# Optimization experiments

Measured on AMD Instinct MI355X. Metric: run time of the kernel, lower is better.

Reference implementation:

```python
import jax, jax.numpy as jnp
import numpy as np

N, E, G = 100000, 1600000, 1000
D_IN, D, L, C = 128, 300, 5, 10


def setup_inputs() -> dict:
    key = jax.random.key(0)
    ks = jax.random.split(key, 32)
    s = 0.05
    inp = {
        'x': jax.random.normal(ks[0], (N, D_IN), jnp.float32),
        'edge_index': jax.random.randint(ks[1], (2, E), 0, N, jnp.int64),
        'batch': jnp.sort(jax.random.randint(ks[2], (N,), 0, G, jnp.int64)),
        'enc_W': jax.random.normal(ks[3], (D_IN, D)) * s,
        'enc_b': jnp.zeros((D,)),
        'eps': jnp.zeros((L,)),
        'cW1': jax.random.normal(ks[4], (L, D, 2 * D)) * s,
        'cb1': jnp.zeros((L, 2 * D)),
        'cbn_s': jnp.ones((L, 2 * D)),
        'cbn_b': jnp.zeros((L, 2 * D)),
        'cW2': jax.random.normal(ks[5], (L, 2 * D, D)) * s,
        'cb2': jnp.zeros((L, D)),
        'bn_s': jnp.ones((L, D)),
        'bn_b': jnp.zeros((L, D)),
        'vn0': jnp.zeros((D,)),
        'vW1': jax.random.normal(ks[6], (L, D, 2 * D)) * s,
        'vb1': jnp.zeros((L, 2 * D)),
        'vbn1_s': jnp.ones((L, 2 * D)),
        'vbn1_b': jnp.zeros((L, 2 * D)),
        'vW2': jax.random.normal(ks[7], (L, 2 * D, D)) * s,
        'vb2': jnp.zeros((L, D)),
        'vbn2_s': jnp.ones((L, D)),
        'vbn2_b': jnp.zeros((L, D)),
        'gW1': jax.random.normal(ks[8], (D, 2 * D)) * s,
        'gb1': jnp.zeros((2 * D,)),
        'gbn_s': jnp.ones((2 * D,)),
        'gbn_b': jnp.zeros((2 * D,)),
        'gW2': jax.random.normal(ks[9], (2 * D, 1)) * s,
        'gb2': jnp.zeros((1,)),
        'pW': jax.random.normal(ks[10], (D, C)) * s,
        'pb': jnp.zeros((C,)),
    }
    return inp


def reference(x, enc_W, enc_b, eps, cW1, cb1, cbn_s, cbn_b, cW2, cb2,
              bn_s, bn_b, vn0, vW1, vb1, vbn1_s, vbn1_b, vW2, vb2,
              vbn2_s, vbn2_b, gW1, gb1, gbn_s, gbn_b, gW2, gb2, pW, pb,
              edge_index, batch):
    src, dst = edge_index[0], edge_index[1]
    n = x.shape[0]
    vn = jnp.broadcast_to(vn0, (G, D))  # virtualnode_embedding(zeros) -> row 0 per graph
    h_list = [x @ enc_W + enc_b]
    for l in range(L):
        hl = h_list[l] + vn[batch]  # virtual-node broadcast gather
        # GIN conv: MLP((1+eps)*h + sum_{j in N(i)} h_j)
        agg = jax.ops.segment_sum(hl[src], dst, num_segments=n)
        t = (1.0 + eps[l]) * hl + agg
        t = jax.nn.relu((t @ cW1[l] + cb1[l]) * cbn_s[l] + cbn_b[l])
        h = (t @ cW2[l] + cb2[l]) * bn_s[l] + bn_b[l]  # layer BN (eval, folded)
        if l < L - 1:
            h = jax.nn.relu(h)  # dropout is identity in eval
        # virtual-node update: global_add_pool + MLP
        vtmp = jax.ops.segment_sum(hl, batch, num_segments=G) + vn
        u = jax.nn.relu((vtmp @ vW1[l] + vb1[l]) * vbn1_s[l] + vbn1_b[l])
        vn = jax.nn.relu((u @ vW2[l] + vb2[l]) * vbn2_s[l] + vbn2_b[l])
        h_list.append(h)
    # JK = 'max' across all L+1 layer outputs
    nr = jnp.max(jnp.stack(h_list, axis=0), axis=0)  # [N, D]
    # GlobalAttention pooling: gate_nn -> per-graph segment softmax
    gate = (jax.nn.relu((nr @ gW1 + gb1) * gbn_s + gbn_b) @ gW2 + gb2)[:, 0]
    gmax = jax.ops.segment_max(gate, batch, num_segments=G)
    e = jnp.exp(gate - gmax[batch])
    denom = jax.ops.segment_sum(e, batch, num_segments=G)
    alpha = e / denom[batch]
    graph_rep = jax.ops.segment_sum(nr * alpha[:, None], batch, num_segments=G)
    return graph_rep @ pW + pb  # [G, C]
```

## Files before the change

kernel.cpp:

```cpp
#include <hip/hip_runtime.h>
#include <cstddef>

#define NGRAPH 1000
#define NEDGES 1600000
#define DD     300
#define DD2    600
#define DIN    128
#define NLAYER 5
#define NCLS   10
#define BR     32
#define BRM    32

#define NT2 38
#define NK2 10
#define NT3 19
#define NK3 19
#define WFRAG 1024
#define W1F_SZ (NT2*NK2*WFRAG)

typedef unsigned short u16;
typedef unsigned char  u8;
typedef unsigned int   u32;
typedef __attribute__((ext_vector_type(8))) short short8;
typedef __attribute__((ext_vector_type(4))) float f32x4;

__device__ __forceinline__ u16 f2bf(float f) {
    u32 u; __builtin_memcpy(&u, &f, 4);
    u = (u + 0x7FFFu + ((u >> 16) & 1u)) >> 16;
    return (u16)u;
}
__device__ __forceinline__ float bf2f(u16 h) {
    u32 u = ((u32)h) << 16;
    float f; __builtin_memcpy(&f, &u, 4); return f;
}

__device__ __forceinline__ float ld24(const u16* __restrict__ hi, const u8* __restrict__ lo,
                                      size_t idx) {
    u32 u = ((u32)hi[idx] << 16) | ((u32)lo[idx] << 8);
    float f; __builtin_memcpy(&f, &u, 4); return f;
}
__device__ __forceinline__ void st24(u16* __restrict__ hi, u8* __restrict__ lo,
                                     size_t idx, float f) {
    u32 u; __builtin_memcpy(&u, &f, 4);
    u32 r = u + 0x7Fu + ((u >> 8) & 1u);
    hi[idx] = (u16)(r >> 16); lo[idx] = (u8)(r >> 8);
}
__device__ __forceinline__ void ld24x4(const u16* __restrict__ hi, const u8* __restrict__ lo,
                                       size_t idx, float o[4]) {
    ushort4 h = *(const ushort4*)(hi + idx);
    uchar4  l = *(const uchar4*)(lo + idx);
    u32 u0 = ((u32)h.x << 16) | ((u32)l.x << 8);
    u32 u1 = ((u32)h.y << 16) | ((u32)l.y << 8);
    u32 u2 = ((u32)h.z << 16) | ((u32)l.z << 8);
    u32 u3 = ((u32)h.w << 16) | ((u32)l.w << 8);
    __builtin_memcpy(&o[0], &u0, 4); __builtin_memcpy(&o[1], &u1, 4);
    __builtin_memcpy(&o[2], &u2, 4); __builtin_memcpy(&o[3], &u3, 4);
}
__device__ __forceinline__ void st24x4(u16* __restrict__ hi, u8* __restrict__ lo,
                                       size_t idx, const float v[4]) {
    u32 u[4];
#pragma unroll
    for (int q = 0; q < 4; ++q) {
        u32 t; __builtin_memcpy(&t, &v[q], 4);
        u[q] = t + 0x7Fu + ((t >> 8) & 1u);
    }
    ushort4 h; h.x = (u16)(u[0] >> 16); h.y = (u16)(u[1] >> 16);
    h.z = (u16)(u[2] >> 16); h.w = (u16)(u[3] >> 16);
    uchar4 l8; l8.x = (u8)(u[0] >> 8); l8.y = (u8)(u[1] >> 8);
    l8.z = (u8)(u[2] >> 8); l8.w = (u8)(u[3] >> 8);
    *(ushort4*)(hi + idx) = h;
    *(uchar4*)(lo + idx) = l8;
}

__global__ void diag_kernel(float* __restrict__ out, int n, float val)
{
    int i = blockIdx.x * 256 + threadIdx.x;
    if (i < n) out[i] = val;
}

__global__ void vn_init_kernel(float* __restrict__ vn, const float* __restrict__ vn0)
{
    int idx = blockIdx.x * 256 + threadIdx.x;
    if (idx < NGRAPH * DD) vn[idx] = vn0[idx % DD];
}

__global__ void bconv_kernel(const int* __restrict__ braw, int n, int* __restrict__ b32)
{
    int i = blockIdx.x * 256 + threadIdx.x;
    if (i >= n) return;
    int fs = (braw[n - 1] == 0) ? 2 : 1;
    b32[i] = braw[(size_t)i * fs];
}

__global__ void packW_kernel(const float* __restrict__ W, int K, int N,
                             int nT, int nK, short* __restrict__ dst)
{
    int idx = blockIdx.x * 256 + threadIdx.x;
    int total = nT * nK * 64;
    if (idx >= total) return;
    int lane = idx & 63;
    int tk = idx >> 6;
    int nn = (tk / nK) * 16 + (lane & 15);
    int k0 = (tk % nK) * 32 + (lane >> 4) * 8;
    short* o = dst + ((size_t)tk << 10) + lane * 8;
#pragma unroll
    for (int j = 0; j < 8; ++j) {
        float v = (nn < N && (k0 + j) < K) ? W[(size_t)(k0 + j) * N + nn] : 0.f;
        u16 h = f2bf(v);
        o[j] = (short)h;
        o[512 + j] = (short)f2bf(v - bf2f(h));
    }
}

__global__ void deg_kernel(const int* __restrict__ ei, int fe, int E, int* __restrict__ deg)
{
    int e = blockIdx.x * 256 + threadIdx.x;
    if (e < E) atomicAdd(&deg[ei[(size_t)fe * (E + e)]], 1);
}

__global__ void scan_kernel(const int* __restrict__ deg, int* __restrict__ row_ptr, int n)
{
    __shared__ int sd[1024];
    int t = threadIdx.x;
    int C = (n + 1023) >> 10;
    int i0 = t * C, i1 = i0 + C; if (i1 > n) i1 = n; if (i0 > n) i0 = n;
    int s = 0;
    for (int i = i0; i < i1; ++i) s += deg[i];
    sd[t] = s;
    __syncthreads();
    for (int o = 1; o < 1024; o <<= 1) {
        int x = (t >= o) ? sd[t - o] : 0;
        __syncthreads();
        sd[t] += x;
        __syncthreads();
    }
    int run = (t == 0) ? 0 : sd[t - 1];
    for (int i = i0; i < i1; ++i) { row_ptr[i] = run; run += deg[i]; }
    if (t == 1023) row_ptr[n] = sd[1023];
}

__global__ void scatter_kernel(const int* __restrict__ ei, int fe, int E,
                               int* __restrict__ cursor, int* __restrict__ col_idx)
{
    int e = blockIdx.x * 256 + threadIdx.x;
    if (e < E) {
        int d = ei[(size_t)fe * (E + e)];
        int s = ei[(size_t)fe * e];
        int p = atomicAdd(&cursor[d], 1);
        col_idx[p] = s;
    }
}

__device__ __forceinline__ int lower_bound_i(const int* __restrict__ arr, int n, int key)
{
    int lo = 0, hi = n;
    while (lo < hi) {
        int mid = (lo + hi) >> 1;
        if (arr[mid] < key) lo = mid + 1; else hi = mid;
    }
    return lo;
}

__global__ void vtmp_kernel(const u16* __restrict__ hi, const u8* __restrict__ lo,
                            const int* __restrict__ batch, const float* __restrict__ vn,
                            float* __restrict__ vtmp, int n)
{
    int g = blockIdx.x, t = threadIdx.x;
    int l0 = lower_bound_i(batch, n, g);
    int h0 = lower_bound_i(batch, n, g + 1);
    if (t >= DD) return;
    float acc = 0.f;
    for (int i = l0; i < h0; ++i) acc += ld24(hi, lo, (size_t)i * DD + t);
    vtmp[(size_t)g * DD + t] = acc + vn[(size_t)g * DD + t];
}

__global__ void vn_mlp_kernel(const float* __restrict__ vtmp,
                              const float* __restrict__ W1, const float* __restrict__ b1,
                              const float* __restrict__ s1, const float* __restrict__ sb1,
                              const float* __restrict__ W2, const float* __restrict__ b2,
                              const float* __restrict__ s2, const float* __restrict__ sb2,
                              float* __restrict__ vn)
{
    __shared__ float vt[DD];
    __shared__ float us[DD2];
    int g = blockIdx.x, t = threadIdx.x;
    if (t < DD) vt[t] = vtmp[(size_t)g * DD + t];
    __syncthreads();
    for (int j = t; j < DD2; j += 512) {
        float acc = 0.f;
        for (int k = 0; k < DD; ++k) acc = fmaf(vt[k], W1[(size_t)k * DD2 + j], acc);
        us[j] = fmaxf(fmaf(acc + b1[j], s1[j], sb1[j]), 0.f);
    }
    __syncthreads();
    for (int j = t; j < DD; j += 512) {
        float acc = 0.f;
        for (int k = 0; k < DD2; ++k) acc = fmaf(us[k], W2[(size_t)k * DD + j], acc);
        vn[(size_t)g * DD + j] = fmaxf(fmaf(acc + b2[j], s2[j], sb2[j]), 0.f);
    }
}

__global__ __launch_bounds__(1024)
void encoder_kernel(const float* __restrict__ x, const float* __restrict__ W,
                    const float* __restrict__ b,
                    u16* __restrict__ Ahi, u8* __restrict__ Alo,
                    short* __restrict__ NRm, float* __restrict__ NRscale, int n)
{
    __shared__ float xs[BR][DIN];
    __shared__ float wmax[16][8];
    __shared__ float rowS[BR];
    const int tid = threadIdx.x;
    const int base = blockIdx.x * BR;
    for (int idx = tid; idx < BR * DIN; idx += 1024) {
        int r = idx >> 7, c = idx & 127;
        int node = base + r;
        xs[r][c] = (node < n) ? x[(size_t)node * DIN + c] : 0.f;
    }
    __syncthreads();
    const int rq = tid >> 8, ct = tid & 255;
    const int wid = tid >> 6, lane = tid & 63;
    const int j0 = ct; const bool has1 = ct < (DD - 256); const int j1 = ct + 256;
    float acc[8][2] = {};
    for (int k = 0; k < DIN; ++k) {
        const float* wr = W + (size_t)k * DD;
        float w0 = wr[j0], w1 = has1 ? wr[j1] : 0.f;
#pragma unroll
        for (int i = 0; i < 8; ++i) {
            float a = xs[rq * 8 + i][k];
            acc[i][0] = fmaf(a, w0, acc[i][0]);
            acc[i][1] = fmaf(a, w1, acc[i][1]);
        }
    }
    float bb0 = b[j0], bb1 = has1 ? b[j1] : 0.f;
    float v0[8], v1[8], lm[8];
#pragma unroll
    for (int i = 0; i < 8; ++i) {
        v0[i] = acc[i][0] + bb0;
        v1[i] = has1 ? (acc[i][1] + bb1) : 0.f;
        lm[i] = fmaxf(fabsf(v0[i]), fabsf(v1[i]));
    }
#pragma unroll
    for (int o = 32; o > 0; o >>= 1)
#pragma unroll
        for (int i = 0; i < 8; ++i) lm[i] = fmaxf(lm[i], __shfl_xor(lm[i], o));
    if (lane == 0)
#pragma unroll
        for (int i = 0; i < 8; ++i) wmax[wid][i] = lm[i];
    __syncthreads();
    if (ct < 8) {
        int r = rq * 8 + ct;
        float m = fmaxf(fmaxf(wmax[4 * rq][ct], wmax[4 * rq + 1][ct]),
                        fmaxf(wmax[4 * rq + 2][ct], wmax[4 * rq + 3][ct]));
        float S = fmaxf(m, 1e-30f) / 32767.f;
        rowS[r] = S;
        if (base + r < n) NRscale[base + r] = S;
    }
    __syncthreads();
#pragma unroll
    for (int i = 0; i < 8; ++i) {
        int r = rq * 8 + i;
        int node = base + r;
        if (node >= n) continue;
        float S = rowS[r];
        size_t idx = (size_t)node * DD + j0;
        st24(Ahi, Alo, idx, v0[i]);
        NRm[idx] = (short)rintf(v0[i] / S);
        if (has1) {
            st24(Ahi, Alo, idx + 256, v1[i]);
            NRm[idx + 256] = (short)rintf(v1[i] / S);
        }
    }
}

__global__ __launch_bounds__(256)
void agg_kernel(const u16* __restrict__ Phi, const u8* __restrict__ Plo,
                u16* __restrict__ Qhi, u8* __restrict__ Qlo,
                const int* __restrict__ row_ptr, const int* __restrict__ col_idx,
                const float* __restrict__ eps, int l, int n)
{
    int node = blockIdx.x * 4 + (threadIdx.x >> 6);
    int lane = threadIdx.x & 63;
    if (node >= n) return;
    const float ep = 1.0f + eps[l];
    const bool two = (lane < 11);
    float a0[4] = {0.f, 0.f, 0.f, 0.f}, a1[4] = {0.f, 0.f, 0.f, 0.f};
    int e0 = row_ptr[node], e1 = row_ptr[node + 1];
    for (int e = e0; e < e1; ++e) {
        int src = col_idx[e];
        size_t rb = (size_t)src * DD;
        float v[4];
        ld24x4(Phi, Plo, rb + lane * 4, v);
        a0[0] += v[0]; a0[1] += v[1]; a0[2] += v[2]; a0[3] += v[3];
        if (two) {
            ld24x4(Phi, Plo, rb + 256 + lane * 4, v);
            a1[0] += v[0]; a1[1] += v[1]; a1[2] += v[2]; a1[3] += v[3];
        }
    }
    size_t ob = (size_t)node * DD;
    float v[4], o[4];
    ld24x4(Phi, Plo, ob + lane * 4, v);
#pragma unroll
    for (int q = 0; q < 4; ++q) o[q] = fmaf(ep, v[q], a0[q]);
    st24x4(Qhi, Qlo, ob + lane * 4, o);
    if (two) {
        ld24x4(Phi, Plo, ob + 256 + lane * 4, v);
#pragma unroll
        for (int q = 0; q < 4; ++q) o[q] = fmaf(ep, v[q], a1[q]);
        st24x4(Qhi, Qlo, ob + 256 + lane * 4, o);
    }
}

__global__ __launch_bounds__(512)
void mlp_kernel(u16* __restrict__ Qhi, u8* __restrict__ Qlo,
                short* __restrict__ NRm, float* __restrict__ NRscale,
                const short* __restrict__ W1f, const float* __restrict__ b1,
                const float* __restrict__ s1, const float* __restrict__ sb1,
                const short* __restrict__ W2f, const float* __restrict__ b2,
                const float* __restrict__ s2, const float* __restrict__ sb2,
                int relu2, const float* __restrict__ vnp,
                const int* __restrict__ batch, int n)
{
    __shared__ char uni[78848];
    __shared__ float rowM[32], rowSo[32], rowSn[32];
    short* agh = (short*)uni;
    short* agl = (short*)(uni + 20992);
    short* tlh = (short*)uni;
    short* tll = (short*)(uni + 39424);
    float* outb = (float*)uni;

    const int tid = threadIdx.x;
    const int base = blockIdx.x * BRM;
    const int wv = tid >> 6, lane = tid & 63;
    const int cl = lane & 15, kq = lane >> 4, r0 = kq * 4;

    for (int idx = tid; idx < 32 * 320; idx += 512) {
        int r = idx / 320, c = idx - r * 320;
        int node = base + r;
        float v = (c < DD && node < n) ? ld24(Qhi, Qlo, (size_t)node * DD + c) : 0.f;
        u16 h = f2bf(v);
        agh[r * 328 + c] = (short)h;
        agl[r * 328 + c] = (short)f2bf(v - bf2f(h));
    }
    __syncthreads();

    {
        f32x4 acc[2][5];
#pragma unroll
        for (int s = 0; s < 2; ++s)
#pragma unroll
            for (int i = 0; i < 5; ++i) acc[s][i] = (f32x4){0.f, 0.f, 0.f, 0.f};
        const bool act5 = (wv + 32) < NT2;
        for (int ks = 0; ks < NK2; ++ks) {
            short8 bh[5], bl[5];
#pragma unroll
            for (int i = 0; i < 5; ++i) {
                int t = wv + 8 * i;
                if (i < 4 || act5) {
                    const short* bp = W1f + (((size_t)t * NK2 + ks) << 10) + lane * 8;
                    bh[i] = *(const short8*)bp;
                    bl[i] = *(const short8*)(bp + 512);
                }
            }
            short8 ah0 = *(const short8*)&agh[cl * 328 + kq * 8 + ks * 32];
            short8 al0 = *(const short8*)&agl[cl * 328 + kq * 8 + ks * 32];
            short8 ah1 = *(const short8*)&agh[(16 + cl) * 328 + kq * 8 + ks * 32];
            short8 al1 = *(const short8*)&agl[(16 + cl) * 328 + kq * 8 + ks * 32];
#pragma unroll
            for (int i = 0; i < 5; ++i)
                if (i < 4 || act5) {
                    acc[0][i] = __builtin_amdgcn_mfma_f32_16x16x32_bf16(ah0, bh[i], acc[0][i], 0, 0, 0);
                    acc[1][i] = __builtin_amdgcn_mfma_f32_16x16x32_bf16(ah1, bh[i], acc[1][i], 0, 0, 0);
                }
#pragma unroll
            for (int i = 0; i < 5; ++i)
                if (i < 4 || act5) {
                    acc[0][i] = __builtin_amdgcn_mfma_f32_16x16x32_bf16(ah0, bl[i], acc[0][i], 0, 0, 0);
                    acc[1][i] = __builtin_amdgcn_mfma_f32_16x16x32_bf16(ah1, bl[i], acc[1][i], 0, 0, 0);
                }
#pragma unroll
            for (int i = 0; i < 5; ++i)
                if (i < 4 || act5) {
                    acc[0][i] = __builtin_amdgcn_mfma_f32_16x16x32_bf16(al0, bh[i], acc[0][i], 0, 0, 0);
                    acc[1][i] = __builtin_amdgcn_mfma_f32_16x16x32_bf16(al1, bh[i], acc[1][i], 0, 0, 0);
                }
        }
        __syncthreads();
        if (tid < 256) {
            int r = tid >> 3, c = 600 + (tid & 7);
            tlh[r * 616 + c] = 0; tll[r * 616 + c] = 0;
        }
#pragma unroll
        for (int s = 0; s < 2; ++s)
#pragma unroll
            for (int i = 0; i < 5; ++i) {
                int t = wv + 8 * i;
                if (t >= NT2) continue;
                int cg = t * 16 + cl;
                if (cg < DD2) {
                    float bb = b1[cg], ss = s1[cg], cc = sb1[cg];
#pragma unroll
                    for (int r = 0; r < 4; ++r) {
                        float xv = fmaxf(fmaf(acc[s][i][r] + bb, ss, cc), 0.f);
                        u16 h = f2bf(xv);
                        tlh[(s * 16 + r0 + r) * 616 + cg] = (short)h;
                        tll[(s * 16 + r0 + r) * 616 + cg] = (short)f2bf(xv - bf2f(h));
                    }
                }
            }
    }
    __syncthreads();

    {
        f32x4 acc[2][3];
#pragma unroll
        for (int s = 0; s < 2; ++s)
#pragma unroll
            for (int i = 0; i < 3; ++i) acc[s][i] = (f32x4){0.f, 0.f, 0.f, 0.f};
        const bool act3 = (wv + 16) < NT3;
        for (int ks = 0; ks < NK3; ++ks) {
            short8 bh[3], bl[3];
#pragma unroll
            for (int i = 0; i < 3; ++i) {
                int t = wv + 8 * i;
                if (i < 2 || act3) {
                    const short* bp = W2f + (((size_t)t * NK3 + ks) << 10) + lane * 8;
                    bh[i] = *(const short8*)bp;
                    bl[i] = *(const short8*)(bp + 512);
                }
            }
            short8 ah0 = *(const short8*)&tlh[cl * 616 + kq * 8 + ks * 32];
            short8 al0 = *(const short8*)&tll[cl * 616 + kq * 8 + ks * 32];
            short8 ah1 = *(const short8*)&tlh[(16 + cl) * 616 + kq * 8 + ks * 32];
            short8 al1 = *(const short8*)&tll[(16 + cl) * 616 + kq * 8 + ks * 32];
#pragma unroll
            for (int i = 0; i < 3; ++i)
                if (i < 2 || act3) {
                    acc[0][i] = __builtin_amdgcn_mfma_f32_16x16x32_bf16(ah0, bh[i], acc[0][i], 0, 0, 0);
                    acc[1][i] = __builtin_amdgcn_mfma_f32_16x16x32_bf16(ah1, bh[i], acc[1][i], 0, 0, 0);
                }
#pragma unroll
            for (int i = 0; i < 3; ++i)
                if (i < 2 || act3) {
                    acc[0][i] = __builtin_amdgcn_mfma_f32_16x16x32_bf16(ah0, bl[i], acc[0][i], 0, 0, 0);
                    acc[1][i] = __builtin_amdgcn_mfma_f32_16x16x32_bf16(ah1, bl[i], acc[1][i], 0, 0, 0);
                }
#pragma unroll
            for (int i = 0; i < 3; ++i)
                if (i < 2 || act3) {
                    acc[0][i] = __builtin_amdgcn_mfma_f32_16x16x32_bf16(al0, bh[i], acc[0][i], 0, 0, 0);
                    acc[1][i] = __builtin_amdgcn_mfma_f32_16x16x32_bf16(al1, bh[i], acc[1][i], 0, 0, 0);
                }
        }
        __syncthreads();
#pragma unroll
        for (int s = 0; s < 2; ++s)
#pragma unroll
            for (int i = 0; i < 3; ++i) {
                int t = wv + 8 * i;
                if (t >= NT3) continue;
                int cg = t * 16 + cl;
#pragma unroll
                for (int r = 0; r < 4; ++r) outb[(s * 16 + r0 + r) * 304 + cg] = acc[s][i][r];
            }
    }
    __syncthreads();

    {
        const int rr = tid >> 4;
        const int qq = tid & 15;
        float lm = 0.f;
        for (int c = qq; c < DD; c += 16) {
            float v = fmaf(outb[rr * 304 + c] + b2[c], s2[c], sb2[c]);
            if (relu2) v = fmaxf(v, 0.f);
            outb[rr * 304 + c] = v;
            lm = fmaxf(lm, fabsf(v));
        }
#pragma unroll
        for (int o = 8; o > 0; o >>= 1) lm = fmaxf(lm, __shfl_xor(lm, o));
        if (qq == 0) rowM[rr] = lm;
        __syncthreads();
        if (tid < 32) {
            int node = base + tid;
            float oS = (node < n) ? NRscale[node] : 0.f;
            float newM = fmaxf(rowM[tid], oS * 32767.f);
            float nS = fmaxf(newM, 1e-30f) / 32767.f;
            rowSo[tid] = oS; rowSn[tid] = nS;
            if (node < n) NRscale[node] = nS;
        }
        __syncthreads();
        int node = base + rr;
        if (node < n) {
            float oS = rowSo[rr], inv = 1.0f / rowSn[rr];
            const float* vrow = vnp ? (vnp + (size_t)batch[node] * DD) : nullptr;
            for (int c = qq; c < DD; c += 16) {
                float v = outb[rr * 304 + c];
                size_t idx = (size_t)node * DD + c;
                float hl = vrow ? (v + vrow[c]) : v;
                st24(Qhi, Qlo, idx, hl);
                float nv = fmaxf((float)NRm[idx] * oS, v);
                NRm[idx] = (short)rintf(nv * inv);
            }
        }
    }
}

__global__ __launch_bounds__(512)
void gate_kernel(const short* __restrict__ NRm, const float* __restrict__ NRscale,
                 const short* __restrict__ W1f, const float* __restrict__ b1,
                 const float* __restrict__ s1, const float* __restrict__ sb1,
                 const float* __restrict__ W2, const float* __restrict__ b2,
                 float* __restrict__ gate, int n)
{
    __shared__ char uni[78336];
    __shared__ float sc[32];
    short* nbh = (short*)uni;
    short* nbl = (short*)(uni + 20992);
    float* tlf = (float*)uni;

    const int tid = threadIdx.x;
    const int base = blockIdx.x * BRM;
    const int wv = tid >> 6, lane = tid & 63;
    const int cl = lane & 15, kq = lane >> 4, r0 = kq * 4;

    if (tid < 32) {
        int node = base + tid;
        sc[tid] = (node < n) ? NRscale[node] : 0.f;
    }
    __syncthreads();
    for (int idx = tid; idx < 32 * 320; idx += 512) {
        int r = idx / 320, c = idx - r * 320;
        int node = base + r;
        float v = (c < DD && node < n) ? (float)NRm[(size_t)node * DD + c] * sc[r] : 0.f;
        u16 h = f2bf(v);
        nbh[r * 328 + c] = (short)h;
        nbl[r * 328 + c] = (short)f2bf(v - bf2f(h));
    }
    __syncthreads();

    {
        f32x4 acc[2][5];
#pragma unroll
        for (int s = 0; s < 2; ++s)
#pragma unroll
            for (int i = 0; i < 5; ++i) acc[s][i] = (f32x4){0.f, 0.f, 0.f, 0.f};
        const bool act5 = (wv + 32) < NT2;
        for (int ks = 0; ks < NK2; ++ks) {
            short8 bh[5], bl[5];
#pragma unroll
            for (int i = 0; i < 5; ++i) {
                int t = wv + 8 * i;
                if (i < 4 || act5) {
                    const short* bp = W1f + (((size_t)t * NK2 + ks) << 10) + lane * 8;
                    bh[i] = *(const short8*)bp;
                    bl[i] = *(const short8*)(bp + 512);
                }
            }
            short8 ah0 = *(const short8*)&nbh[cl * 328 + kq * 8 + ks * 32];
            short8 al0 = *(const short8*)&nbl[cl * 328 + kq * 8 + ks * 32];
            short8 ah1 = *(const short8*)&nbh[(16 + cl) * 328 + kq * 8 + ks * 32];
            short8 al1 = *(const short8*)&nbl[(16 + cl) * 328 + kq * 8 + ks * 32];
#pragma unroll
            for (int i = 0; i < 5; ++i)
                if (i < 4 || act5) {
                    acc[0][i] = __builtin_amdgcn_mfma_f32_16x16x32_bf16(ah0, bh[i], acc[0][i], 0, 0, 0);
                    acc[1][i] = __builtin_amdgcn_mfma_f32_16x16x32_bf16(ah1, bh[i], acc[1][i], 0, 0, 0);
                }
#pragma unroll
            for (int i = 0; i < 5; ++i)
                if (i < 4 || act5) {
                    acc[0][i] = __builtin_amdgcn_mfma_f32_16x16x32_bf16(ah0, bl[i], acc[0][i], 0, 0, 0);
                    acc[1][i] = __builtin_amdgcn_mfma_f32_16x16x32_bf16(ah1, bl[i], acc[1][i], 0, 0, 0);
                }
#pragma unroll
            for (int i = 0; i < 5; ++i)
                if (i < 4 || act5) {
                    acc[0][i] = __builtin_amdgcn_mfma_f32_16x16x32_bf16(al0, bh[i], acc[0][i], 0, 0, 0);
                    acc[1][i] = __builtin_amdgcn_mfma_f32_16x16x32_bf16(al1, bh[i], acc[1][i], 0, 0, 0);
                }
        }
        __syncthreads();
#pragma unroll
        for (int s = 0; s < 2; ++s)
#pragma unroll
            for (int i = 0; i < 5; ++i) {
                int t = wv + 8 * i;
                if (t >= NT2) continue;
                int cg = t * 16 + cl;
                if (cg < DD2) {
                    float bb = b1[cg], ss = s1[cg], cc = sb1[cg];
#pragma unroll
                    for (int r = 0; r < 4; ++r)
                        tlf[(s * 16 + r0 + r) * 612 + cg] = fmaxf(fmaf(acc[s][i][r] + bb, ss, cc), 0.f);
                }
            }
    }
    __syncthreads();

    {
        const int wave = tid >> 6, ln = tid & 63;
#pragma unroll
        for (int rr = 0; rr < 4; ++rr) {
            int r = wave * 4 + rr;
            int node = base + r;
            float acc = 0.f;
            for (int j = ln; j < DD2; j += 64) acc = fmaf(tlf[r * 612 + j], W2[j], acc);
#pragma unroll
            for (int o = 32; o > 0; o >>= 1) acc += __shfl_down(acc, o);
            if (ln == 0 && node < n) gate[node] = acc + b2[0];
        }
    }
}

__global__ void attn_pool_kernel(const float* __restrict__ gate,
                                 const short* __restrict__ NRm, const float* __restrict__ NRscale,
                                 const int* __restrict__ batch, float* __restrict__ rep, int n)
{
    __shared__ float red[320];
    __shared__ float bc[2];
    int g = blockIdx.x, t = threadIdx.x;
    int l0 = lower_bound_i(batch, n, g);
    int h0 = lower_bound_i(batch, n, g + 1);
    if (l0 >= h0) { if (t < DD) rep[(size_t)g * DD + t] = 0.f; return; }

    float m = -3.4e38f;
    for (int i = l0 + t; i < h0; i += 320) m = fmaxf(m, gate[i]);
    red[t] = m;
    __syncthreads();
    if (t < 64) {
        float mm = red[t];
        for (int s2 = t + 64; s2 < 320; s2 += 64) mm = fmaxf(mm, red[s2]);
#pragma unroll
        for (int o = 32; o > 0; o >>= 1) mm = fmaxf(mm, __shfl_down(mm, o));
        if (t == 0) bc[0] = mm;
    }
    __syncthreads();
    float gmax = bc[0];

    float ssum = 0.f;
    for (int i = l0 + t; i < h0; i += 320) ssum += expf(gate[i] - gmax);
    __syncthreads();
    red[t] = ssum;
    __syncthreads();
    if (t < 64) {
        float mm = red[t];
        for (int s2 = t + 64; s2 < 320; s2 += 64) mm += red[s2];
#pragma unroll
        for (int o = 32; o > 0; o >>= 1) mm += __shfl_down(mm, o);
        if (t == 0) bc[1] = mm;
    }
    __syncthreads();
    float inv = 1.0f / bc[1];

    if (t < DD) {
        float acc = 0.f;
        for (int i = l0; i < h0; ++i) {
            float w = expf(gate[i] - gmax) * inv;
            acc = fmaf(w, (float)NRm[(size_t)i * DD + t] * NRscale[i], acc);
        }
        rep[(size_t)g * DD + t] = acc;
    }
}

__global__ void final_kernel(const float* __restrict__ rep, const float* __restrict__ pW,
                             const float* __restrict__ pb, float* __restrict__ out)
{
    int g = blockIdx.x, lane = threadIdx.x;
    float a[NCLS] = {};
    for (int d = lane; d < DD; d += 64) {
        float r = rep[(size_t)g * DD + d];
#pragma unroll
        for (int c = 0; c < NCLS; ++c) a[c] = fmaf(r, pW[d * NCLS + c], a[c]);
    }
#pragma unroll
    for (int c = 0; c < NCLS; ++c) {
#pragma unroll
        for (int o = 32; o > 0; o >>= 1) a[c] += __shfl_down(a[c], o);
    }
    if (lane == 0) {
#pragma unroll
        for (int c = 0; c < NCLS; ++c) out[g * NCLS + c] = a[c] + pb[c];
    }
}

extern "C" void kernel_launch(void* const* d_in, const int* in_sizes, int n_in,
                              void* d_out, int out_size, void* d_ws, size_t ws_size,
                              hipStream_t stream)
{
    (void)n_in;
    const float* x      = (const float*)d_in[0];
    const int*   ei     = (const int*)d_in[1];
    const int*   braw   = (const int*)d_in[2];
    const float* enc_W  = (const float*)d_in[3];
    const float* enc_b  = (const float*)d_in[4];
    const float* eps    = (const float*)d_in[5];
    const float* cW1    = (const float*)d_in[6];
    const float* cb1    = (const float*)d_in[7];
    const float* cbn_s  = (const float*)d_in[8];
    const float* cbn_b  = (const float*)d_in[9];
    const float* cW2    = (const float*)d_in[10];
    const float* cb2    = (const float*)d_in[11];
    const float* bn_s   = (const float*)d_in[12];
    const float* bn_b   = (const float*)d_in[13];
    const float* vn0    = (const float*)d_in[14];
    const float* vW1    = (const float*)d_in[15];
    const float* vb1    = (const float*)d_in[16];
    const float* vbn1_s = (const float*)d_in[17];
    const float* vbn1_b = (const float*)d_in[18];
    const float* vW2    = (const float*)d_in[19];
    const float* vb2    = (const float*)d_in[20];
    const float* vbn2_s = (const float*)d_in[21];
    const float* vbn2_b = (const float*)d_in[22];
    const float* gW1    = (const float*)d_in[23];
    const float* gb1    = (const float*)d_in[24];
    const float* gbn_s  = (const float*)d_in[25];
    const float* gbn_b  = (const float*)d_in[26];
    const float* gW2    = (const float*)d_in[27];
    const float* gb2    = (const float*)d_in[28];
    const float* pW     = (const float*)d_in[29];
    const float* pb     = (const float*)d_in[30];
    float* out = (float*)d_out;

    const int N = in_sizes[0] / DIN;
    const int E = NEDGES;
    int fe = in_sizes[1] / (2 * E);
    if (fe < 1) fe = 1; if (fe > 2) fe = 2;

    char* wsp = (char*)d_ws;
    size_t off = 0;
    auto carve = [&](size_t nbytes) -> void* {
        void* p = (void*)(wsp + off);
        off += ((nbytes + 255) / 256) * 256;
        return p;
    };
    u16*   Ahi     = (u16*)  carve((size_t)N * DD * 2);
    u8*    Alo     = (u8*)   carve((size_t)N * DD);
    u16*   Bhi     = (u16*)  carve((size_t)N * DD * 2);
    u8*    Blo     = (u8*)   carve((size_t)N * DD);
    short* NRm     = (short*)carve((size_t)N * DD * 2);
    float* NRscale = (float*)carve((size_t)N * 4);
    float* vnBuf   = (float*)carve((size_t)NGRAPH * DD * 4);
    float* vtmpBuf = (float*)carve((size_t)NGRAPH * DD * 4);
    float* repBuf  = (float*)carve((size_t)NGRAPH * DD * 4);
    float* gateBuf = (float*)carve((size_t)N * 4);
    int*   batch32 = (int*)  carve((size_t)N * 4);
    int*   row_ptr = (int*)  carve(((size_t)N + 1) * 4);
    int*   cursor  = (int*)  carve((size_t)N * 4);
    int*   col_idx = (int*)  carve((size_t)E * 4);
    short* W1f     = (short*)carve((size_t)NLAYER * W1F_SZ * 2);
    short* W2f     = (short*)carve((size_t)NLAYER * W1F_SZ * 2);
    short* gW1f    = (short*)carve((size_t)W1F_SZ * 2);

    if (off > ws_size) {
        diag_kernel<<<(out_size + 255) / 256, 256, 0, stream>>>(out, out_size, (float)ws_size);
        return;
    }

    const int pkBlocks = (NT2 * NK2 * 64 + 255) / 256;
    for (int l = 0; l < NLAYER; ++l) {
        packW_kernel<<<pkBlocks, 256, 0, stream>>>(cW1 + (size_t)l * DD * DD2, DD, DD2,
                                                   NT2, NK2, W1f + (size_t)l * W1F_SZ);
        packW_kernel<<<pkBlocks, 256, 0, stream>>>(cW2 + (size_t)l * DD2 * DD, DD2, DD,
                                                   NT3, NK3, W2f + (size_t)l * W1F_SZ);
    }
    packW_kernel<<<pkBlocks, 256, 0, stream>>>(gW1, DD, DD2, NT2, NK2, gW1f);

    bconv_kernel<<<(N + 255) / 256, 256, 0, stream>>>(braw, N, batch32);

    (void)hipMemsetAsync(cursor, 0, (size_t)N * 4, stream);
    deg_kernel<<<(E + 255) / 256, 256, 0, stream>>>(ei, fe, E, cursor);
    scan_kernel<<<1, 1024, 0, stream>>>(cursor, row_ptr, N);
    (void)hipMemcpyAsync(cursor, row_ptr, (size_t)N * 4, hipMemcpyDeviceToDevice, stream);
    scatter_kernel<<<(E + 255) / 256, 256, 0, stream>>>(ei, fe, E, cursor, col_idx);

    vn_init_kernel<<<(NGRAPH * DD + 255) / 256, 256, 0, stream>>>(vnBuf, vn0);

    const int nblk32 = (N + BR - 1) / BR;
    const int nblkM  = (N + BRM - 1) / BRM;
    const int nblk4  = (N + 3) / 4;

    encoder_kernel<<<nblk32, 1024, 0, stream>>>(x, enc_W, enc_b, Ahi, Alo, NRm, NRscale, N);

    u16 *Phi = Ahi, *Qhi = Bhi; u8 *Plo = Alo, *Qlo = Blo;
    for (int l = 0; l < NLAYER; ++l) {
        const bool hasVn = (l < NLAYER - 1);
        if (hasVn)
            vtmp_kernel<<<NGRAPH, 320, 0, stream>>>(Phi, Plo, batch32, vnBuf, vtmpBuf, N);
        agg_kernel<<<nblk4, 256, 0, stream>>>(Phi, Plo, Qhi, Qlo, row_ptr, col_idx, eps, l, N);
        if (hasVn)
            vn_mlp_kernel<<<NGRAPH, 512, 0, stream>>>(
                vtmpBuf,
                vW1 + (size_t)l * DD * DD2, vb1 + (size_t)l * DD2,
                vbn1_s + (size_t)l * DD2, vbn1_b + (size_t)l * DD2,
                vW2 + (size_t)l * DD2 * DD, vb2 + (size_t)l * DD,
                vbn2_s + (size_t)l * DD, vbn2_b + (size_t)l * DD,
                vnBuf);
        mlp_kernel<<<nblkM, 512, 0, stream>>>(
            Qhi, Qlo, NRm, NRscale,
            W1f + (size_t)l * W1F_SZ, cb1 + (size_t)l * DD2,
            cbn_s + (size_t)l * DD2, cbn_b + (size_t)l * DD2,
            W2f + (size_t)l * W1F_SZ, cb2 + (size_t)l * DD,
            bn_s + (size_t)l * DD, bn_b + (size_t)l * DD,
            hasVn ? 1 : 0,
            hasVn ? vnBuf : (const float*)nullptr, batch32, N);
        u16* th = Phi; Phi = Qhi; Qhi = th;
        u8*  tb = Plo; Plo = Qlo; Qlo = tb;
    }

    gate_kernel<<<nblkM, 512, 0, stream>>>(NRm, NRscale, gW1f, gb1, gbn_s, gbn_b,
                                           gW2, gb2, gateBuf, N);
    attn_pool_kernel<<<NGRAPH, 320, 0, stream>>>(gateBuf, NRm, NRscale, batch32, repBuf, N);
    final_kernel<<<NGRAPH, 64, 0, stream>>>(repBuf, pW, pb, out);
}
```

Before: 4.445 ms.

## Vectorize tile loads/stores, skip final-layer h write, unroll vtmp reduction

The mlp and gate kernels now load their input tiles and write the epilogue four elements at a time, with short4/float4 vector accesses in place of scalar per-element traffic. The mlp epilogue is restructured so each thread handles four contiguous columns, and the split hi/lo h buffer is no longer written in the last layer, where nothing reads it. The vtmp per-graph reduction uses four independent accumulators to expose more memory-level parallelism. Together these aim to cut global memory transactions and latency-bound loops, at the cost of slightly different fp summation order in vtmp.

```diff
diff --git a/kernel.cpp b/kernel.cpp
--- a/kernel.cpp
+++ b/kernel.cpp
@@ -22,6 +22,7 @@
 typedef unsigned char  u8;
 typedef unsigned int   u32;
 typedef __attribute__((ext_vector_type(8))) short short8;
+typedef __attribute__((ext_vector_type(4))) short short4v;
 typedef __attribute__((ext_vector_type(4))) float f32x4;
 
 __device__ __forceinline__ u16 f2bf(float f) {
@@ -169,9 +170,16 @@
     int l0 = lower_bound_i(batch, n, g);
     int h0 = lower_bound_i(batch, n, g + 1);
     if (t >= DD) return;
-    float acc = 0.f;
-    for (int i = l0; i < h0; ++i) acc += ld24(hi, lo, (size_t)i * DD + t);
-    vtmp[(size_t)g * DD + t] = acc + vn[(size_t)g * DD + t];
+    float a0 = 0.f, a1 = 0.f, a2 = 0.f, a3 = 0.f;
+    int i = l0;
+    for (; i + 3 < h0; i += 4) {
+        a0 += ld24(hi, lo, (size_t)(i + 0) * DD + t);
+        a1 += ld24(hi, lo, (size_t)(i + 1) * DD + t);
+        a2 += ld24(hi, lo, (size_t)(i + 2) * DD + t);
+        a3 += ld24(hi, lo, (size_t)(i + 3) * DD + t);
+    }
+    for (; i < h0; ++i) a0 += ld24(hi, lo, (size_t)i * DD + t);
+    vtmp[(size_t)g * DD + t] = ((a0 + a1) + (a2 + a3)) + vn[(size_t)g * DD + t];
 }
 
 __global__ void vn_mlp_kernel(const float* __restrict__ vtmp,
@@ -317,7 +325,7 @@
                 const short* __restrict__ W2f, const float* __restrict__ b2,
                 const float* __restrict__ s2, const float* __restrict__ sb2,
                 int relu2, const float* __restrict__ vnp,
-                const int* __restrict__ batch, int n)
+                const int* __restrict__ batch, int writeQ, int n)
 {
     __shared__ char uni[78848];
     __shared__ float rowM[32], rowSo[32], rowSn[32];
@@ -332,13 +340,20 @@
     const int wv = tid >> 6, lane = tid & 63;
     const int cl = lane & 15, kq = lane >> 4, r0 = kq * 4;
 
-    for (int idx = tid; idx < 32 * 320; idx += 512) {
-        int r = idx / 320, c = idx - r * 320;
+    for (int idx = tid; idx < 32 * 80; idx += 512) {
+        int r = idx / 80, c4 = (idx - r * 80) * 4;
         int node = base + r;
-        float v = (c < DD && node < n) ? ld24(Qhi, Qlo, (size_t)node * DD + c) : 0.f;
-        u16 h = f2bf(v);
-        agh[r * 328 + c] = (short)h;
-        agl[r * 328 + c] = (short)f2bf(v - bf2f(h));
+        float v[4] = {0.f, 0.f, 0.f, 0.f};
+        if (c4 < DD && node < n) ld24x4(Qhi, Qlo, (size_t)node * DD + c4, v);
+        short4v hh, ll;
+#pragma unroll
+        for (int q = 0; q < 4; ++q) {
+            u16 h = f2bf(v[q]);
+            hh[q] = (short)h;
+            ll[q] = (short)f2bf(v[q] - bf2f(h));
+        }
+        *(short4v*)&agh[r * 328 + c4] = hh;
+        *(short4v*)&agl[r * 328 + c4] = ll;
     }
     __syncthreads();
 
@@ -477,29 +492,45 @@
 #pragma unroll
         for (int o = 8; o > 0; o >>= 1) lm = fmaxf(lm, __shfl_xor(lm, o));
         if (qq == 0) rowM[rr] = lm;
-        __syncthreads();
-        if (tid < 32) {
-            int node = base + tid;
-            float oS = (node < n) ? NRscale[node] : 0.f;
-            float newM = fmaxf(rowM[tid], oS * 32767.f);
-            float nS = fmaxf(newM, 1e-30f) / 32767.f;
-            rowSo[tid] = oS; rowSn[tid] = nS;
-            if (node < n) NRscale[node] = nS;
-        }
-        __syncthreads();
-        int node = base + rr;
-        if (node < n) {
-            float oS = rowSo[rr], inv = 1.0f / rowSn[rr];
-            const float* vrow = vnp ? (vnp + (size_t)batch[node] * DD) : nullptr;
-            for (int c = qq; c < DD; c += 16) {
-                float v = outb[rr * 304 + c];
-                size_t idx = (size_t)node * DD + c;
-                float hl = vrow ? (v + vrow[c]) : v;
-                st24(Qhi, Qlo, idx, hl);
-                float nv = fmaxf((float)NRm[idx] * oS, v);
-                NRm[idx] = (short)rintf(nv * inv);
+    }
+    __syncthreads();
+    if (tid < 32) {
+        int node = base + tid;
+        float oS = (node < n) ? NRscale[node] : 0.f;
+        float newM = fmaxf(rowM[tid], oS * 32767.f);
+        float nS = fmaxf(newM, 1e-30f) / 32767.f;
+        rowSo[tid] = oS; rowSn[tid] = nS;
+        if (node < n) NRscale[node] = nS;
+    }
+    __syncthreads();
+    for (int idx = tid; idx < 32 * 75; idx += 512) {
+        int r = idx / 75, c = (idx - r * 75) * 4;
+        int node = base + r;
+        if (node >= n) continue;
+        float oS = rowSo[r], inv = 1.0f / rowSn[r];
+        size_t gidx = (size_t)node * DD + c;
+        float h0 = outb[r * 304 + c + 0];
+        float h1 = outb[r * 304 + c + 1];
+        float h2 = outb[r * 304 + c + 2];
+        float h3 = outb[r * 304 + c + 3];
+        if (writeQ) {
+            float hl[4];
+            if (vnp) {
+                const float* vrow = vnp + (size_t)batch[node] * DD;
+                float4 vv = *(const float4*)(vrow + c);
+                hl[0] = h0 + vv.x; hl[1] = h1 + vv.y; hl[2] = h2 + vv.z; hl[3] = h3 + vv.w;
+            } else {
+                hl[0] = h0; hl[1] = h1; hl[2] = h2; hl[3] = h3;
             }
-        }
+            st24x4(Qhi, Qlo, gidx, hl);
+        }
+        short4v old = *(const short4v*)&NRm[gidx];
+        short4v nw;
+        nw[0] = (short)rintf(fmaxf((float)old[0] * oS, h0) * inv);
+        nw[1] = (short)rintf(fmaxf((float)old[1] * oS, h1) * inv);
+        nw[2] = (short)rintf(fmaxf((float)old[2] * oS, h2) * inv);
+        nw[3] = (short)rintf(fmaxf((float)old[3] * oS, h3) * inv);
+        *(short4v*)&NRm[gidx] = nw;
     }
 }
 
@@ -526,13 +557,25 @@
         sc[tid] = (node < n) ? NRscale[node] : 0.f;
     }
     __syncthreads();
-    for (int idx = tid; idx < 32 * 320; idx += 512) {
-        int r = idx / 320, c = idx - r * 320;
+    for (int idx = tid; idx < 32 * 80; idx += 512) {
+        int r = idx / 80, c4 = (idx - r * 80) * 4;
         int node = base + r;
-        float v = (c < DD && node < n) ? (float)NRm[(size_t)node * DD + c] * sc[r] : 0.f;
-        u16 h = f2bf(v);
-        nbh[r * 328 + c] = (short)h;
-        nbl[r * 328 + c] = (short)f2bf(v - bf2f(h));
+        float v[4] = {0.f, 0.f, 0.f, 0.f};
+        if (c4 < DD && node < n) {
+            short4v m4 = *(const short4v*)&NRm[(size_t)node * DD + c4];
+            float s = sc[r];
+            v[0] = (float)m4[0] * s; v[1] = (float)m4[1] * s;
+            v[2] = (float)m4[2] * s; v[3] = (float)m4[3] * s;
+        }
+        short4v hh, ll;
+#pragma unroll
+        for (int q = 0; q < 4; ++q) {
+            u16 h = f2bf(v[q]);
+            hh[q] = (short)h;
+            ll[q] = (short)f2bf(v[q] - bf2f(h));
+        }
+        *(short4v*)&nbh[r * 328 + c4] = hh;
+        *(short4v*)&nbl[r * 328 + c4] = ll;
     }
     __syncthreads();
 
@@ -800,7 +843,8 @@
             W2f + (size_t)l * W1F_SZ, cb2 + (size_t)l * DD,
             bn_s + (size_t)l * DD, bn_b + (size_t)l * DD,
             hasVn ? 1 : 0,
-            hasVn ? vnBuf : (const float*)nullptr, batch32, N);
+            hasVn ? vnBuf : (const float*)nullptr, batch32,
+            hasVn ? 1 : 0, N);
         u16* th = Phi; Phi = Qhi; Qhi = th;
         u8*  tb = Plo; Plo = Qlo; Qlo = tb;
     }
```

Measured after the change: 3.985 ms. 1.12x faster.
